# Optimization experiments

Hardware: AMD Instinct MI355X
Metric: run time of the kernel (lower is better)

Reference implementation:

```python
import jax, jax.numpy as jnp
import numpy as np

B, T = 64, 512
V, E = 512, 128      # dsl vocab, embedding dim
IMG = 1024           # img_repr_size
H = 512              # dsl_hidden_dim
A = 512              # n_actions
PAD = 0


def setup_inputs() -> dict:
    key = jax.random.key(0)
    ks = jax.random.split(key, 10)
    x1 = jax.random.normal(ks[0], (B, IMG), dtype=jnp.float32)
    x2 = jax.random.randint(ks[1], (B, T), 0, V)
    x2_lens = jax.random.randint(ks[2], (B,), 1, T + 1)
    s_in = 1.0 / np.sqrt(E + IMG)
    s_h = 1.0 / np.sqrt(H)
    emb = jax.random.normal(ks[3], (V, E), dtype=jnp.float32)
    emb = emb.at[PAD].set(0.0)  # padding_idx row is zero
    W_ih = jax.random.uniform(ks[4], (4 * H, E + IMG), jnp.float32, -s_h, s_h)
    W_hh = jax.random.uniform(ks[5], (4 * H, H), jnp.float32, -s_h, s_h)
    b_ih = jax.random.uniform(ks[6], (4 * H,), jnp.float32, -s_h, s_h)
    b_hh = jax.random.uniform(ks[7], (4 * H,), jnp.float32, -s_h, s_h)
    W_act = jax.random.uniform(ks[8], (A, H), jnp.float32, -s_h, s_h)
    b_act = jax.random.uniform(ks[9], (A,), jnp.float32, -s_h, s_h)
    return {"x1": x1, "x2": x2, "x2_lens": x2_lens, "emb": emb,
            "W_ih": W_ih, "W_hh": W_hh, "b_ih": b_ih, "b_hh": b_hh,
            "W_act": W_act, "b_act": b_act}


def reference(x1, x2, x2_lens, emb, W_ih, W_hh, b_ih, b_hh, W_act, b_act):
    # embed tokens and concat image repr at every timestep: [B, T, IMG+E]
    tok = emb[x2]                                        # [B, T, E]
    img = jnp.broadcast_to(x1[:, None, :], (B, T, IMG))  # [B, T, IMG]
    x = jnp.concatenate([img, tok], axis=2)              # [B, T, IMG+E]

    # precompute input-to-gate projections in one big GEMM
    gx = jnp.einsum('bti,gi->tbg', x, W_ih) + b_ih       # [T, B, 4H]

    def step(carry, gx_t):
        h, c = carry
        g = gx_t + h @ W_hh.T + b_hh                     # [B, 4H]
        i, f, gg, o = jnp.split(g, 4, axis=1)            # torch gate order i,f,g,o
        i = jax.nn.sigmoid(i); f = jax.nn.sigmoid(f)
        gg = jnp.tanh(gg); o = jax.nn.sigmoid(o)
        c = f * c + i * gg
        h = o * jnp.tanh(c)
        return (h, c), h

    h0 = jnp.zeros((B, H), jnp.float32)
    c0 = jnp.zeros((B, H), jnp.float32)
    (_, _), hs = jax.lax.scan(step, (h0, c0), gx)        # hs: [T, B, H]

    # hn = hidden state at each sequence's true last step (packed-seq semantics)
    idx = (x2_lens - 1).astype(jnp.int32)                # [B]
    hn = jnp.take_along_axis(hs.transpose(1, 0, 2), idx[:, None, None], axis=1)[:, 0, :]  # [B, H]

    nt = hn @ W_act.T + b_act                            # [B, A]
    return nt
```

## Files before the change

### kernel.cpp

```cpp
#include <hip/hip_runtime.h>
#include <cstdint>
#include <cstddef>


typedef _Float16     f16x8 __attribute__((ext_vector_type(8)));
typedef _Float16     f16x2 __attribute__((ext_vector_type(2)));
typedef float        f32x4 __attribute__((ext_vector_type(4)));
typedef float        f32x2 __attribute__((ext_vector_type(2)));
typedef unsigned int u32x4 __attribute__((ext_vector_type(4)));

#define TPB 256
#define NWG 64

#define WS_GX0   0
#define WS_P     524288
#define WS_HN    4718592
#define WS_HBUF  4849664
#define WS_FLAGS 4980736

__device__ __forceinline__ float sigm_(float x) { return 1.f / (1.f + __expf(-x)); }
__device__ __forceinline__ float tanh_(float x) {
    const float e = __expf(-2.f * fabsf(x));
    return copysignf((1.f - e) / (1.f + e), x);
}

__device__ __forceinline__ void st_ic_u32(unsigned int* p, unsigned int v) {
    __hip_atomic_store(p, v, __ATOMIC_RELAXED, __HIP_MEMORY_SCOPE_AGENT);
}
__device__ __forceinline__ unsigned int ld_ic_u32(const unsigned int* p) {
    return __hip_atomic_load(p, __ATOMIC_RELAXED, __HIP_MEMORY_SCOPE_AGENT);
}

__global__ void gemm_nt_bias(const float* __restrict__ A, int lda,
                             const float* __restrict__ B, int ldb,
                             float* __restrict__ C, int ldc, int K,
                             const float* __restrict__ bias1,
                             const float* __restrict__ bias2)
{
    __shared__ float As[32 * 68];
    __shared__ float Bs[32 * 68];
    const int tid = threadIdx.x;
    const int m0 = blockIdx.y * 64, n0 = blockIdx.x * 64;
    const int kchunk = K / gridDim.z;
    const int kbeg = blockIdx.z * kchunk, kend = kbeg + kchunk;
    const int tr = tid >> 4, tc = tid & 15;
    float acc[4][4] = {};

    for (int k0 = kbeg; k0 < kend; k0 += 32) {
        __syncthreads();
        #pragma unroll
        for (int idx = tid; idx < 2048; idx += TPB) {
            const int r = idx >> 5, kk = idx & 31;
            As[kk * 68 + r] = A[(size_t)(m0 + r) * lda + k0 + kk];
            Bs[kk * 68 + r] = B[(size_t)(n0 + r) * ldb + k0 + kk];
        }
        __syncthreads();
        #pragma unroll
        for (int kk = 0; kk < 32; ++kk) {
            const f32x4 a = *(const f32x4*)&As[kk * 68 + tr * 4];
            const f32x4 b = *(const f32x4*)&Bs[kk * 68 + tc * 4];
            #pragma unroll
            for (int i = 0; i < 4; ++i)
                #pragma unroll
                for (int j = 0; j < 4; ++j)
                    acc[i][j] = fmaf(a[i], b[j], acc[i][j]);
        }
    }

    const bool split = (gridDim.z > 1);
    #pragma unroll
    for (int i = 0; i < 4; ++i) {
        const int m = m0 + tr * 4 + i;
        #pragma unroll
        for (int j = 0; j < 4; ++j) {
            const int n = n0 + tc * 4 + j;
            float v = acc[i][j];
            if (blockIdx.z == 0) {
                if (bias1) v += bias1[n];
                if (bias2) v += bias2[n];
            }
            if (split) atomicAdd(&C[(size_t)m * ldc + n], v);
            else       C[(size_t)m * ldc + n] = v;
        }
    }
}

__global__ void __launch_bounds__(TPB, 1)
lstm_seq(const float* __restrict__ Whh,
         const float* __restrict__ GX0,
         const float* __restrict__ P,
         const int*   __restrict__ x2,
         const int*   __restrict__ lens,
         _Float16*    hbuf,
         float*       __restrict__ hn,
         unsigned int* flags)
{
    __shared__ float Spart[4 * 128 * 20];

    const int tid = threadIdx.x, wg = blockIdx.x;
    const int lane = tid & 63, wv = tid >> 6;
    const int BG = wg >> 4;
    const int CG = wg & 15;
    const int m16 = lane & 15, q = lane >> 4;

    const int bl  = tid >> 4;
    const int cq  = (tid & 15) * 2;
    const int b   = BG * 16 + bl;
    const int col = CG * 32 + cq;
    const int last = lens[b] - 1;
    const int* toks = x2 + b * 512;

    f32x2 gxv[4];
    {
        const float* gx = GX0 + (size_t)b * 2048 + col;
        #pragma unroll
        for (int g = 0; g < 4; ++g) gxv[g] = *(const f32x2*)(gx + g * 512);
    }

    { f16x2 z; z[0] = (_Float16)0.f; z[1] = (_Float16)0.f;
      st_ic_u32((unsigned int*)(hbuf + b * 512 + col),
                __builtin_bit_cast(unsigned int, z)); }
    __syncthreads();
    unsigned int* myflag = flags + (size_t)wg * 64;
    if (tid == 0) st_ic_u32(myflag, 1u);

    const unsigned int* pollp =
        flags + (size_t)(BG * 16 + wv * 4 + (lane & 3)) * 64;

    f16x8 bfr[8][4];
    #pragma unroll
    for (int n = 0; n < 8; ++n) {
        const int rr = n * 16 + m16;
        const int gr = (rr >> 5) * 512 + CG * 32 + (rr & 31);
        const float* wrow = Whh + (size_t)gr * 512 + wv * 128 + q * 8;
        #pragma unroll
        for (int ks = 0; ks < 4; ++ks) {
            const f32x4 w0 = *(const f32x4*)(wrow + ks * 32);
            const f32x4 w1 = *(const f32x4*)(wrow + ks * 32 + 4);
            f16x8 bv;
            #pragma unroll
            for (int e = 0; e < 4; ++e) {
                bv[e]     = (_Float16)w0[e];
                bv[4 + e] = (_Float16)w1[e];
            }
            bfr[n][ks] = bv;
        }
    }

    int tok1;
    f32x2 ppv[4];
    {
        const int tok0 = toks[0];
        const float* pp = P + (size_t)tok0 * 2048 + col;
        #pragma unroll
        for (int g = 0; g < 4; ++g) ppv[g] = *(const f32x2*)(pp + g * 512);
        tok1 = toks[1];
    }

    float c0 = 0.f, c1 = 0.f;

    for (int t = 0; t < 512; ++t) {
        const unsigned int tgt = (unsigned int)(t + 1);

        while (true) {
            const unsigned int v = ld_ic_u32(pollp);
            if (__all((int)(v >= tgt))) break;
        }
        asm volatile("" ::: "memory");

        const _Float16* hsrc = hbuf + (size_t)(t & 1) * (64 * 512);
        _Float16*       hdst = hbuf + (size_t)((t + 1) & 1) * (64 * 512);

        u32x4 a0, a1, a2, a3;
        {
            const _Float16* ap =
                hsrc + (BG * 16 + m16) * 512 + wv * 128 + q * 8;
            asm volatile(
                "global_load_dwordx4 %0, %4, off sc1\n\t"
                "global_load_dwordx4 %1, %4, off offset:64 sc1\n\t"
                "global_load_dwordx4 %2, %4, off offset:128 sc1\n\t"
                "global_load_dwordx4 %3, %4, off offset:192 sc1\n\t"
                "s_waitcnt vmcnt(0)"
                : "=&v"(a0), "=&v"(a1), "=&v"(a2), "=&v"(a3)
                : "v"(ap)
                : "memory");
        }
        f16x8 af[4] = {
            __builtin_bit_cast(f16x8, a0), __builtin_bit_cast(f16x8, a1),
            __builtin_bit_cast(f16x8, a2), __builtin_bit_cast(f16x8, a3)
        };

        f32x4 acc[8] = {};
        #pragma unroll
        for (int ks = 0; ks < 4; ++ks)
            #pragma unroll
            for (int n = 0; n < 8; ++n)
                acc[n] = __builtin_amdgcn_mfma_f32_16x16x32_f16(
                    af[ks], bfr[n][ks], acc[n], 0, 0, 0);

        {
            const int cl = lane & 15, gq = lane >> 4;
            #pragma unroll
            for (int n = 0; n < 8; ++n) {
                const int row = wv * 128 + n * 16 + cl;
                *(f32x4*)&Spart[row * 20 + ((gq + (row >> 3)) & 3) * 4] = acc[n];
            }
        }
        __syncthreads();

        f32x2 sv[4];
        #pragma unroll
        for (int g = 0; g < 4; ++g) {
            f32x2 s = {0.f, 0.f};
            #pragma unroll
            for (int w = 0; w < 4; ++w) {
                const int r0 = w * 128 + g * 32 + cq;
                const int base =
                    r0 * 20 + (((bl >> 2) + (r0 >> 3)) & 3) * 4 + (bl & 3);
                s[0] += Spart[base];
                s[1] += Spart[base + 20];
            }
            sv[g] = s;
        }

        float hv[2];
        #pragma unroll
        for (int p = 0; p < 2; ++p) {
            const float iv = sigm_(sv[0][p] + gxv[0][p] + ppv[0][p]);
            const float fv = sigm_(sv[1][p] + gxv[1][p] + ppv[1][p]);
            const float gv = tanh_(sv[2][p] + gxv[2][p] + ppv[2][p]);
            const float ov = sigm_(sv[3][p] + gxv[3][p] + ppv[3][p]);
            float& c = p ? c1 : c0;
            c = fv * c + iv * gv;
            hv[p] = ov * tanh_(c);
        }

        f16x2 hh; hh[0] = (_Float16)hv[0]; hh[1] = (_Float16)hv[1];
        st_ic_u32((unsigned int*)(hdst + b * 512 + col),
                  __builtin_bit_cast(unsigned int, hh));
        if (t == last) {
            f32x2 o; o[0] = hv[0]; o[1] = hv[1];
            *(f32x2*)(hn + (size_t)b * 512 + col) = o;
        }

        __syncthreads();
        if (tid == 0) st_ic_u32(myflag, (unsigned int)(t + 2));

        {
            const float* pn = P + (size_t)tok1 * 2048 + col;
            #pragma unroll
            for (int g = 0; g < 4; ++g)
                ppv[g] = *(const f32x2*)(pn + g * 512);
            tok1 = toks[t < 510 ? t + 2 : 511];
        }
    }
}

extern "C" void kernel_launch(void* const* d_in, const int* in_sizes, int n_in,
                              void* d_out, int out_size, void* d_ws, size_t ws_size,
                              hipStream_t stream)
{
    const float* x1    = (const float*)d_in[0];
    const int*   x2    = (const int*)  d_in[1];
    const int*   lens  = (const int*)  d_in[2];
    const float* emb   = (const float*)d_in[3];
    const float* W_ih  = (const float*)d_in[4];
    const float* W_hh  = (const float*)d_in[5];
    const float* b_ih  = (const float*)d_in[6];
    const float* b_hh  = (const float*)d_in[7];
    const float* W_act = (const float*)d_in[8];
    const float* b_act = (const float*)d_in[9];
    float* out = (float*)d_out;

    char* ws = (char*)d_ws;
    float*        GX0   = (float*)(ws + WS_GX0);
    float*        P     = (float*)(ws + WS_P);
    float*        hn    = (float*)(ws + WS_HN);
    _Float16*     hbuf  = (_Float16*)(ws + WS_HBUF);
    unsigned int* flags = (unsigned int*)(ws + WS_FLAGS);

    hipMemsetAsync(flags, 0, 16384, stream);
    hipMemsetAsync(GX0, 0, 64 * 2048 * sizeof(float), stream);
    hipMemsetAsync(out, 0, 64 * 512 * sizeof(float), stream);

    gemm_nt_bias<<<dim3(32, 1, 4), TPB, 0, stream>>>(
        x1, 1024, W_ih, 1152, GX0, 2048, 1024, b_ih, b_hh);
    gemm_nt_bias<<<dim3(32, 8, 1), TPB, 0, stream>>>(
        emb, 128, W_ih + 1024, 1152, P, 2048, 128, nullptr, nullptr);

    lstm_seq<<<NWG, TPB, 0, stream>>>(W_hh, GX0, P, x2, lens, hbuf, hn, flags);

    gemm_nt_bias<<<dim3(8, 1, 4), TPB, 0, stream>>>(
        hn, 512, W_act, 512, out, 512, 512, b_act, nullptr);
}
```

Baseline: 1.375 ms.

## Merge prologue GEMMs, fuse output projection into LSTM, pipeline flag polling

The two input-projection GEMMs are merged into one launch by dispatching on block index. The final action projection moves into the tail of the recurrent kernel: each workgroup waits on the flags of its batch group, loads hn into LDS and computes its output slice directly. This removes the output memset and two launches. The per-step flag poll becomes hand-written asm that keeps two loads in flight with an s_sleep, trading some extra memory traffic for lower wake-up latency.

```diff
diff --git a/kernel.cpp b/kernel.cpp
--- a/kernel.cpp
+++ b/kernel.cpp
@@ -30,19 +30,43 @@
 __device__ __forceinline__ unsigned int ld_ic_u32(const unsigned int* p) {
     return __hip_atomic_load(p, __ATOMIC_RELAXED, __HIP_MEMORY_SCOPE_AGENT);
 }
-
-__global__ void gemm_nt_bias(const float* __restrict__ A, int lda,
-                             const float* __restrict__ B, int ldb,
-                             float* __restrict__ C, int ldc, int K,
-                             const float* __restrict__ bias1,
-                             const float* __restrict__ bias2)
+__device__ __forceinline__ void st_ic_u64(unsigned long long* p, unsigned long long v) {
+    __hip_atomic_store(p, v, __ATOMIC_RELAXED, __HIP_MEMORY_SCOPE_AGENT);
+}
+
+__global__ void __launch_bounds__(TPB, 1)
+gemm_prologue(const float* __restrict__ x1,
+              const float* __restrict__ emb,
+              const float* __restrict__ W_ih,
+              const float* __restrict__ b_ih,
+              const float* __restrict__ b_hh,
+              float* __restrict__ GX0,
+              float* __restrict__ P)
 {
     __shared__ float As[32 * 68];
     __shared__ float Bs[32 * 68];
     const int tid = threadIdx.x;
-    const int m0 = blockIdx.y * 64, n0 = blockIdx.x * 64;
-    const int kchunk = K / gridDim.z;
-    const int kbeg = blockIdx.z * kchunk, kend = kbeg + kchunk;
+    const int bid = blockIdx.x;
+
+    const float *A, *B, *bias1 = nullptr, *bias2 = nullptr;
+    float* C;
+    int lda, ldb, ldc, m0, n0, kbeg, kend;
+    bool split;
+    if (bid < 128) {
+        const int z = bid >> 5;
+        A = x1;  lda = 1024; B = W_ih; ldb = 1152;
+        C = GX0; ldc = 2048;
+        m0 = 0; n0 = (bid & 31) * 64;
+        kbeg = z * 256; kend = kbeg + 256; split = true;
+        if (z == 0) { bias1 = b_ih; bias2 = b_hh; }
+    } else {
+        const int t2 = bid - 128;
+        A = emb; lda = 128; B = W_ih + 1024; ldb = 1152;
+        C = P;   ldc = 2048;
+        m0 = (t2 >> 5) * 64; n0 = (t2 & 31) * 64;
+        kbeg = 0; kend = 128; split = false;
+    }
+
     const int tr = tid >> 4, tc = tid & 15;
     float acc[4][4] = {};
 
@@ -67,7 +91,6 @@
         }
     }
 
-    const bool split = (gridDim.z > 1);
     #pragma unroll
     for (int i = 0; i < 4; ++i) {
         const int m = m0 + tr * 4 + i;
@@ -75,10 +98,8 @@
         for (int j = 0; j < 4; ++j) {
             const int n = n0 + tc * 4 + j;
             float v = acc[i][j];
-            if (blockIdx.z == 0) {
-                if (bias1) v += bias1[n];
-                if (bias2) v += bias2[n];
-            }
+            if (bias1) v += bias1[n];
+            if (bias2) v += bias2[n];
             if (split) atomicAdd(&C[(size_t)m * ldc + n], v);
             else       C[(size_t)m * ldc + n] = v;
         }
@@ -92,8 +113,11 @@
          const int*   __restrict__ x2,
          const int*   __restrict__ lens,
          _Float16*    hbuf,
-         float*       __restrict__ hn,
-         unsigned int* flags)
+         float*       hn,
+         unsigned int* flags,
+         const float* __restrict__ W_act,
+         const float* __restrict__ b_act,
+         float*       __restrict__ out)
 {
     __shared__ float Spart[4 * 128 * 20];
 
@@ -162,11 +186,25 @@
     for (int t = 0; t < 512; ++t) {
         const unsigned int tgt = (unsigned int)(t + 1);
 
-        while (true) {
-            const unsigned int v = ld_ic_u32(pollp);
-            if (__all((int)(v >= tgt))) break;
-        }
-        asm volatile("" ::: "memory");
+        unsigned int f0, f1;
+        asm volatile(
+            "global_load_dword %0, %2, off sc1\n\t"
+            "s_sleep 8\n\t"
+            "global_load_dword %1, %2, off sc1\n\t"
+            "Lpoll%=:\n\t"
+            "s_waitcnt vmcnt(1)\n\t"
+            "v_cmp_lt_u32 vcc, %0, %3\n\t"
+            "s_cbranch_vccz Ldone%=\n\t"
+            "global_load_dword %0, %2, off sc1\n\t"
+            "s_waitcnt vmcnt(1)\n\t"
+            "v_cmp_lt_u32 vcc, %1, %3\n\t"
+            "s_cbranch_vccz Ldone%=\n\t"
+            "global_load_dword %1, %2, off sc1\n\t"
+            "s_branch Lpoll%=\n\t"
+            "Ldone%=:\n\t"
+            : "=&v"(f0), "=&v"(f1)
+            : "v"(pollp), "v"(tgt)
+            : "memory", "vcc");
 
         const _Float16* hsrc = hbuf + (size_t)(t & 1) * (64 * 512);
         _Float16*       hdst = hbuf + (size_t)((t + 1) & 1) * (64 * 512);
@@ -182,7 +220,7 @@
                 "global_load_dwordx4 %3, %4, off offset:192 sc1\n\t"
                 "s_waitcnt vmcnt(0)"
                 : "=&v"(a0), "=&v"(a1), "=&v"(a2), "=&v"(a3)
-                : "v"(ap)
+                : "v"(ap), "v"(f0), "v"(f1)
                 : "memory");
         }
         f16x8 af[4] = {
@@ -240,7 +278,8 @@
                   __builtin_bit_cast(unsigned int, hh));
         if (t == last) {
             f32x2 o; o[0] = hv[0]; o[1] = hv[1];
-            *(f32x2*)(hn + (size_t)b * 512 + col) = o;
+            st_ic_u64((unsigned long long*)(hn + (size_t)b * 512 + col),
+                      __builtin_bit_cast(unsigned long long, o));
         }
 
         __syncthreads();
@@ -253,6 +292,61 @@
                 ppv[g] = *(const f32x2*)(pn + g * 512);
             tok1 = toks[t < 510 ? t + 2 : 511];
         }
+    }
+
+    {
+        const unsigned int* ep = flags + (size_t)(BG * 16 + (lane & 15)) * 64;
+        while (true) {
+            const unsigned int v = ld_ic_u32(ep);
+            if (__all((int)(v >= 513u))) break;
+        }
+        asm volatile("" ::: "memory");
+
+        float* hnL = Spart;
+        {
+            const int r  = tid >> 4;
+            const int c0 = (tid & 15) * 4;
+            const float* src = hn + (size_t)(BG * 16 + r) * 512 + c0;
+            float* dst = hnL + r * 516 + c0;
+            u32x4 d0, d1, d2, d3, d4, d5, d6, d7;
+            asm volatile(
+                "global_load_dwordx4 %0, %8, off sc1\n\t"
+                "global_load_dwordx4 %1, %8, off offset:256 sc1\n\t"
+                "global_load_dwordx4 %2, %8, off offset:512 sc1\n\t"
+                "global_load_dwordx4 %3, %8, off offset:768 sc1\n\t"
+                "global_load_dwordx4 %4, %8, off offset:1024 sc1\n\t"
+                "global_load_dwordx4 %5, %8, off offset:1280 sc1\n\t"
+                "global_load_dwordx4 %6, %8, off offset:1536 sc1\n\t"
+                "global_load_dwordx4 %7, %8, off offset:1792 sc1\n\t"
+                "s_waitcnt vmcnt(0)"
+                : "=&v"(d0), "=&v"(d1), "=&v"(d2), "=&v"(d3),
+                  "=&v"(d4), "=&v"(d5), "=&v"(d6), "=&v"(d7)
+                : "v"(src)
+                : "memory");
+            *(u32x4*)(dst)       = d0; *(u32x4*)(dst + 64)  = d1;
+            *(u32x4*)(dst + 128) = d2; *(u32x4*)(dst + 192) = d3;
+            *(u32x4*)(dst + 256) = d4; *(u32x4*)(dst + 320) = d5;
+            *(u32x4*)(dst + 384) = d6; *(u32x4*)(dst + 448) = d7;
+        }
+        __syncthreads();
+
+        const float* w0 = W_act + (size_t)col * 512;
+        const float* w1 = w0 + 512;
+        float s0 = b_act[col], s1 = b_act[col + 1];
+        const float* h = hnL + bl * 516;
+        #pragma unroll 4
+        for (int k = 0; k < 512; k += 4) {
+            const f32x4 hv4 = *(const f32x4*)(h + k);
+            const f32x4 wa  = *(const f32x4*)(w0 + k);
+            const f32x4 wb  = *(const f32x4*)(w1 + k);
+            #pragma unroll
+            for (int e = 0; e < 4; ++e) {
+                s0 = fmaf(hv4[e], wa[e], s0);
+                s1 = fmaf(hv4[e], wb[e], s1);
+            }
+        }
+        f32x2 o; o[0] = s0; o[1] = s1;
+        *(f32x2*)(out + (size_t)b * 512 + col) = o;
     }
 }
 
@@ -281,15 +375,10 @@
 
     hipMemsetAsync(flags, 0, 16384, stream);
     hipMemsetAsync(GX0, 0, 64 * 2048 * sizeof(float), stream);
-    hipMemsetAsync(out, 0, 64 * 512 * sizeof(float), stream);
-
-    gemm_nt_bias<<<dim3(32, 1, 4), TPB, 0, stream>>>(
-        x1, 1024, W_ih, 1152, GX0, 2048, 1024, b_ih, b_hh);
-    gemm_nt_bias<<<dim3(32, 8, 1), TPB, 0, stream>>>(
-        emb, 128, W_ih + 1024, 1152, P, 2048, 128, nullptr, nullptr);
-
-    lstm_seq<<<NWG, TPB, 0, stream>>>(W_hh, GX0, P, x2, lens, hbuf, hn, flags);
-
-    gemm_nt_bias<<<dim3(8, 1, 4), TPB, 0, stream>>>(
-        hn, 512, W_act, 512, out, 512, 512, b_act, nullptr);
-}
+
+    gemm_prologue<<<dim3(384), TPB, 0, stream>>>(
+        x1, emb, W_ih, b_ih, b_hh, GX0, P);
+
+    lstm_seq<<<NWG, TPB, 0, stream>>>(W_hh, GX0, P, x2, lens, hbuf, hn, flags,
+                                      W_act, b_act, out);
+}
```

Measured after the change: 1.347 ms. 2.0% less time.
